# Kernel optimization log

Measured on AMD Instinct MI355X. Metric: run time of the kernel, lower is better.

The kernel has to match this reference:

```python
import jax, jax.numpy as jnp
import numpy as np

N = 100000
E = 1600000
IN_C = 128
OUT_C = 32
HEADS = 4
NEG_SLOPE = 0.2


def setup_inputs() -> dict:
    key = jax.random.key(0)
    k1, k2, k3, k4, k5 = jax.random.split(key, 5)
    x = jax.random.normal(k1, (N, IN_C), dtype=jnp.float32)
    edge_index = jax.random.randint(k2, (2, E), 0, N, dtype=jnp.int64)
    # Xavier-ish scaled params
    W = jax.random.normal(k3, (OUT_C * HEADS, IN_C), dtype=jnp.float32) * (1.414 * np.sqrt(2.0 / (IN_C + OUT_C * HEADS)))
    att_l = jax.random.normal(k4, (1, HEADS, OUT_C), dtype=jnp.float32) * 0.1
    att_r = jax.random.normal(k5, (1, HEADS, OUT_C), dtype=jnp.float32) * 0.1
    bias = jnp.zeros((OUT_C * HEADS,), dtype=jnp.float32)
    return {"x": x, "edge_index": edge_index, "W": W, "att_l": att_l, "att_r": att_r, "bias": bias}


def reference(x, edge_index, W, att_l, att_r, bias):
    row, col = edge_index[0], edge_index[1]
    # per-node projection: [N, H, C]
    x_proj = (x @ W.T).reshape(N, HEADS, OUT_C)
    x_i = x_proj[row]          # [E, H, C] gather by source
    x_j = x_proj[col]          # [E, H, C] gather by target
    alpha = (x_i * att_l).sum(-1) + (x_j * att_r).sum(-1)   # [E, H]
    alpha = jnp.where(alpha >= 0, alpha, NEG_SLOPE * alpha)  # leaky_relu
    # edge softmax grouped by row (faithful: plain exp, eps=1e-16)
    alpha_exp = jnp.exp(alpha)
    denom = jax.ops.segment_sum(alpha_exp, row, num_segments=N)  # [N, H]
    alpha = alpha_exp / (denom[row] + 1e-16)
    # weighted scatter-add over all heads at once: [N, H, C]
    out = jax.ops.segment_sum(x_j * alpha[:, :, None], row, num_segments=N)
    out = out.reshape(N, HEADS * OUT_C) + bias
    return out
```

## Files before the change

kernel.cpp:

```cpp
#include <hip/hip_runtime.h>
#include <hip/hip_fp16.h>


constexpr float NEG_SLOPE = 0.2f;
constexpr int TILE_ROWS = 64;
constexpr int SLAB = 2048;
constexpr int EPB = 8192;
constexpr int NB_PAD = 2048;
constexpr int FBMAX = 256;

typedef __attribute__((ext_vector_type(8))) short short8;
typedef __attribute__((ext_vector_type(4))) float f32x4;

__device__ inline short f2bf(float f) {
    unsigned u = __float_as_uint(f);
    return (short)((u + 0x7fffu + ((u >> 16) & 1u)) >> 16);
}

__global__ __launch_bounds__(512) void k_fg(const float* __restrict__ x,
                                            const float* __restrict__ W,
                                            const float* __restrict__ attl,
                                            const float* __restrict__ attr,
                                            const int* __restrict__ ei,
                                            __half* __restrict__ xph,
                                            float* __restrict__ l,
                                            float* __restrict__ r,
                                            unsigned int* __restrict__ slab,
                                            int* __restrict__ starts,
                                            int N, int E, int NB, int FB, int S) {
    __shared__ __align__(16) char smem[49152];
    __shared__ float s_att[256];
    __shared__ int s_wsum[8];
    int t = threadIdx.x;
    int lane = t & 63, wv = t >> 6;
    int b = blockIdx.x;
    bool isfill = (b % S == 0) && (b / S < FB);

    if (isfill) {
        int* s_hist = (int*)smem;
        int* s_cur  = (int*)(smem + 8192);
        unsigned int* s_stage = (unsigned int*)(smem + 16384);

        int fb = b / S;
        int e0 = fb * EPB;
        int ecnt = min(EPB, E - e0);
        bool full = (ecnt == EPB) && ((E & 3) == 0);

        for (int i = t; i < NB_PAD; i += 512) s_hist[i] = 0;
        __syncthreads();

        const int* rows = ei;
        const int* cols = ei + E;

        if (full) {
            const int4* r4 = (const int4*)rows + (e0 >> 2);
#pragma unroll
            for (int k = 0; k < 4; ++k) {
                int4 ra = r4[k * 512 + t];
                atomicAdd(&s_hist[ra.x >> 6], 1);
                atomicAdd(&s_hist[ra.y >> 6], 1);
                atomicAdd(&s_hist[ra.z >> 6], 1);
                atomicAdd(&s_hist[ra.w >> 6], 1);
            }
        } else {
            for (int j = t; j < ecnt; j += 512)
                atomicAdd(&s_hist[rows[e0 + j] >> 6], 1);
        }
        __syncthreads();

        int b0 = t * 4;
        int c0 = s_hist[b0], c1 = s_hist[b0 + 1], c2 = s_hist[b0 + 2], c3 = s_hist[b0 + 3];
        int p = c0 + c1 + c2 + c3;
        int v = p;
#pragma unroll
        for (int off = 1; off < 64; off <<= 1) {
            int u = __shfl_up(v, off);
            if (lane >= off) v += u;
        }
        if (lane == 63) s_wsum[wv] = v;
        __syncthreads();
        if (t == 0) {
            int run = 0;
#pragma unroll
            for (int w = 0; w < 8; ++w) { int tmp = s_wsum[w]; s_wsum[w] = run; run += tmp; }
        }
        __syncthreads();
        int base = s_wsum[wv] + (v - p);
        int e1 = base + c0, e2 = e1 + c1, e3 = e2 + c2;
        s_hist[b0] = base; s_hist[b0 + 1] = e1; s_hist[b0 + 2] = e2; s_hist[b0 + 3] = e3;
        s_cur[b0] = base;  s_cur[b0 + 1] = e1;  s_cur[b0 + 2] = e2;  s_cur[b0 + 3] = e3;
        size_t sb = (size_t)fb * (NB + 1);
        if (b0 + 0 <= NB) starts[sb + b0 + 0] = base;
        if (b0 + 1 <= NB) starts[sb + b0 + 1] = e1;
        if (b0 + 2 <= NB) starts[sb + b0 + 2] = e2;
        if (b0 + 3 <= NB) starts[sb + b0 + 3] = e3;
        __syncthreads();

        if (full) {
            const int4* r4 = (const int4*)rows + (e0 >> 2);
            const int4* c4 = (const int4*)cols + (e0 >> 2);
#pragma unroll
            for (int k = 0; k < 4; ++k) {
                int4 ra = r4[k * 512 + t];
                int4 ca = c4[k * 512 + t];
                int pos;
                pos = atomicAdd(&s_cur[ra.x >> 6], 1);
                s_stage[pos] = ((unsigned int)ca.x << 6) | (unsigned int)(ra.x & 63);
                pos = atomicAdd(&s_cur[ra.y >> 6], 1);
                s_stage[pos] = ((unsigned int)ca.y << 6) | (unsigned int)(ra.y & 63);
                pos = atomicAdd(&s_cur[ra.z >> 6], 1);
                s_stage[pos] = ((unsigned int)ca.z << 6) | (unsigned int)(ra.z & 63);
                pos = atomicAdd(&s_cur[ra.w >> 6], 1);
                s_stage[pos] = ((unsigned int)ca.w << 6) | (unsigned int)(ra.w & 63);
            }
        } else {
            for (int j = t; j < ecnt; j += 512) {
                int rr = rows[e0 + j], cc = cols[e0 + j];
                int pos = atomicAdd(&s_cur[rr >> 6], 1);
                s_stage[pos] = ((unsigned int)cc << 6) | (unsigned int)(rr & 63);
            }
        }
        __syncthreads();

        uint4* dst = (uint4*)(slab + (size_t)fb * EPB);
        const uint4* src = (const uint4*)s_stage;
        int n4 = (ecnt + 3) >> 2;
        for (int i = t; i < n4; i += 512) dst[i] = src[i];
        return;
    }

    short* s_wa = (short*)smem;
    if (t < 128)       s_att[t] = attl[t];
    else if (t < 256)  s_att[t] = attr[t - 128];
    for (int i = t; i < 128 * 128; i += 512) {
        int row = i >> 7, col = i & 127;
        s_wa[row * 136 + col] = f2bf(W[i]);
    }
    for (int i = t; i < 1024; i += 512) {
        int row = 136 + (i >> 7), col = i & 127;
        s_wa[row * 136 + col] = 0;
    }
    __syncthreads();
#pragma unroll
    for (int s = 0; s < 2; ++s) {
        int e = t + s * 512;
        int which = e >> 9;
        int h = (e >> 7) & 3;
        int k = e & 127;
        float acc = 0.f;
#pragma unroll 8
        for (int c = 0; c < 32; ++c)
            acc += s_att[which * 128 + h * 32 + c] * W[(h * 32 + c) * 128 + k];
        s_wa[(128 + which * 4 + h) * 136 + k] = f2bf(acc);
    }
    __syncthreads();

    int li = lane & 15, quad = lane >> 4;
    int gb = b - min((b + S - 1) / S, FB);
    int base = gb * 128 + wv * 16;

    f32x4 acc[9];
#pragma unroll
    for (int nt = 0; nt < 9; ++nt) acc[nt] = (f32x4){0.f, 0.f, 0.f, 0.f};

    int anode = base + li;
    bool avalid = anode < N;
    const float4* x4 = (const float4*)x;
    const short8* wb8 = (const short8*)s_wa;

#pragma unroll
    for (int kc = 0; kc < 4; ++kc) {
        float4 p0 = make_float4(0.f, 0.f, 0.f, 0.f), p1 = p0;
        if (avalid) {
            p0 = x4[(size_t)anode * 32 + kc * 8 + quad * 2];
            p1 = x4[(size_t)anode * 32 + kc * 8 + quad * 2 + 1];
        }
        short8 a;
        a[0] = f2bf(p0.x); a[1] = f2bf(p0.y); a[2] = f2bf(p0.z); a[3] = f2bf(p0.w);
        a[4] = f2bf(p1.x); a[5] = f2bf(p1.y); a[6] = f2bf(p1.z); a[7] = f2bf(p1.w);
#pragma unroll
        for (int nt = 0; nt < 9; ++nt) {
            short8 bfrag = wb8[(nt * 16 + li) * 17 + kc * 4 + quad];
            acc[nt] = __builtin_amdgcn_mfma_f32_16x16x32_bf16(a, bfrag, acc[nt], 0, 0, 0);
        }
    }

#pragma unroll
    for (int j = 0; j < 4; ++j) {
        int node = base + quad * 4 + j;
        if (node >= N) continue;
        if (li < 4)      l[node * 4 + li] = acc[8][j];
        else if (li < 8) r[node * 4 + li - 4] = acc[8][j];
    }

    __syncthreads();
    __half* s_out = (__half*)s_wa;
#pragma unroll
    for (int j = 0; j < 4; ++j) {
        int nl = wv * 16 + quad * 4 + j;
#pragma unroll
        for (int nt = 0; nt < 8; ++nt)
            s_out[nl * 136 + nt * 16 + li] = __float2half(acc[nt][j]);
    }
    __syncthreads();
    {
        int nl = t >> 2, seg = t & 3;
        int node = gb * 128 + nl;
        if (node < N) {
            const short8* sr = (const short8*)s_wa;
            short8* xp8 = (short8*)xph;
#pragma unroll
            for (int q = 0; q < 4; ++q)
                xp8[(size_t)node * 16 + seg * 4 + q] = sr[nl * 17 + seg * 4 + q];
        }
    }
}

__global__ __launch_bounds__(512, 8) void k_tile(const int* __restrict__ starts,
                                                 const unsigned int* __restrict__ slab,
                                                 const float* __restrict__ l,
                                                 const float* __restrict__ r,
                                                 const __half* __restrict__ xph,
                                                 const float* __restrict__ bias,
                                                 float* __restrict__ out,
                                                 int N, int NB, int FB) {
    __shared__ int s_col[SLAB];
    __shared__ __half s_w[SLAB * 4];
    __shared__ float s_dsum[TILE_ROWS * 4];
    __shared__ float s_l[TILE_ROWS * 4];
    __shared__ int s_start[TILE_ROWS + 1];
    __shared__ int s_cursor[TILE_ROWS];
    __shared__ int s_cnt[TILE_ROWS];
    __shared__ int s_fbase[FBMAX];
    __shared__ int s_foff[FBMAX + 1];
    __shared__ int s_w4[4];

    int b = blockIdx.x;
    int base = b * TILE_ROWS;
    int t = threadIdx.x;
    int lane = t & 63, wv = t >> 6;
    int rows = min(TILE_ROWS, N - base);

    if (t < TILE_ROWS) s_cnt[t] = 0;
    if (t < rows * 4) s_l[t] = l[base * 4 + t];

    int myc = 0;
    if (t < FB) {
        const int* sp = starts + (size_t)t * (NB + 1) + b;
        int a0 = sp[0], a1 = sp[1];
        s_fbase[t] = a0;
        myc = a1 - a0;
    }
    if (t < 256) {
        int v = myc;
#pragma unroll
        for (int off = 1; off < 64; off <<= 1) {
            int u = __shfl_up(v, off);
            if (lane >= off) v += u;
        }
        if (lane == 63) s_w4[wv] = v;
        s_foff[t + 1] = v;
    }
    __syncthreads();
    if (t == 0) {
        int run = 0;
#pragma unroll
        for (int w = 0; w < 4; ++w) { int tmp = s_w4[w]; s_w4[w] = run; run += tmp; }
        s_foff[0] = 0;
    }
    __syncthreads();
    if (t < 256) s_foff[t + 1] += s_w4[wv];
    __syncthreads();
    int tot = s_foff[FB];
    if (tot > SLAB) tot = SLAB;

    unsigned int pk[4];
#pragma unroll
    for (int s = 0; s < 4; ++s) {
        int i = t + s * 512;
        pk[s] = 0xFFFFFFFFu;
        if (i < tot) {
            int lo = 0, hi = FB;
            while (hi - lo > 1) {
                int mid = (lo + hi) >> 1;
                if (s_foff[mid] <= i) lo = mid; else hi = mid;
            }
            pk[s] = slab[(size_t)lo * EPB + s_fbase[lo] + (i - s_foff[lo])];
        }
    }
#pragma unroll
    for (int s = 0; s < 4; ++s)
        if (pk[s] != 0xFFFFFFFFu) atomicAdd(&s_cnt[pk[s] & 63], 1);
    __syncthreads();

    if (t < 64) {
        int c = s_cnt[t];
        int vv = c;
#pragma unroll
        for (int off = 1; off < 64; off <<= 1) {
            int u = __shfl_up(vv, off);
            if (t >= off) vv += u;
        }
        s_start[t + 1] = vv;
        if (t == 0) s_start[0] = 0;
        s_cursor[t] = vv - c;
    }
    __syncthreads();

    {
        int row_[4], col_[4];
#pragma unroll
        for (int s = 0; s < 4; ++s) {
            row_[s] = (int)(pk[s] & 63);
            col_[s] = (pk[s] != 0xFFFFFFFFu) ? (int)(pk[s] >> 6) : 0;
        }
        float4 rv[4];
#pragma unroll
        for (int s = 0; s < 4; ++s) rv[s] = ((const float4*)r)[col_[s]];
#pragma unroll
        for (int s = 0; s < 4; ++s) {
            if (pk[s] == 0xFFFFFFFFu) continue;
            int row = row_[s];
            int pos = atomicAdd(&s_cursor[row], 1);
            s_col[pos] = col_[s];
            float4 lv = ((const float4*)s_l)[row];
            float w0 = lv.x + rv[s].x, w1 = lv.y + rv[s].y;
            float w2 = lv.z + rv[s].z, w3 = lv.w + rv[s].w;
            w0 = w0 >= 0.f ? w0 : NEG_SLOPE * w0;
            w1 = w1 >= 0.f ? w1 : NEG_SLOPE * w1;
            w2 = w2 >= 0.f ? w2 : NEG_SLOPE * w2;
            w3 = w3 >= 0.f ? w3 : NEG_SLOPE * w3;
            w0 = __expf(w0); w1 = __expf(w1); w2 = __expf(w2); w3 = __expf(w3);
            ((__half2*)s_w)[pos * 2]     = __floats2half2_rn(w0, w1);
            ((__half2*)s_w)[pos * 2 + 1] = __floats2half2_rn(w2, w3);
        }
    }
    __syncthreads();

    if (t < 256) {
        int row = t >> 2, h = t & 3;
        if (row < rows) {
            int s0 = s_start[row], s1 = s_start[row + 1];
            float d = 0.f;
            for (int i = s0; i < s1; ++i)
                d += __half2float(s_w[i * 4 + h]);
            s_dsum[t] = d;
        }
    }
    __syncthreads();

    int quarter = lane >> 4;
    int li = lane & 15;
    int h = li >> 2;
    const float4* xp4g = (const float4*)xph;

    float4 b0 = ((const float4*)bias)[2 * li];
    float4 b1 = ((const float4*)bias)[2 * li + 1];

    for (int rl = wv; rl < rows; rl += 8) {
        int s0 = s_start[rl], s1 = s_start[rl + 1];
        float a0 = 0.f, a1 = 0.f, a2 = 0.f, a3 = 0.f;
        float a4 = 0.f, a5 = 0.f, a6 = 0.f, a7 = 0.f;
        for (int i0 = s0 + quarter; i0 < s1; i0 += 16) {
            int i1 = i0 + 4, i2 = i0 + 8, i3 = i0 + 12;
            bool v1 = i1 < s1, v2 = i2 < s1, v3 = i3 < s1;
            int c0 = s_col[i0];
            int c1 = v1 ? s_col[i1] : c0;
            int c2 = v2 ? s_col[i2] : c0;
            int c3 = v3 ? s_col[i3] : c0;
            float w0 = __half2float(s_w[i0 * 4 + h]);
            float w1 = v1 ? __half2float(s_w[i1 * 4 + h]) : 0.f;
            float w2 = v2 ? __half2float(s_w[i2 * 4 + h]) : 0.f;
            float w3 = v3 ? __half2float(s_w[i3 * 4 + h]) : 0.f;
            float4 r0 = xp4g[(size_t)c0 * 16 + li];
            float4 r1 = xp4g[(size_t)c1 * 16 + li];
            float4 r2 = xp4g[(size_t)c2 * 16 + li];
            float4 r3 = xp4g[(size_t)c3 * 16 + li];
#define ACC8(raw, w)                                             \
            {                                                    \
                const __half* hp = (const __half*)&(raw);        \
                a0 = fmaf((w), __half2float(hp[0]), a0);         \
                a1 = fmaf((w), __half2float(hp[1]), a1);         \
                a2 = fmaf((w), __half2float(hp[2]), a2);         \
                a3 = fmaf((w), __half2float(hp[3]), a3);         \
                a4 = fmaf((w), __half2float(hp[4]), a4);         \
                a5 = fmaf((w), __half2float(hp[5]), a5);         \
                a6 = fmaf((w), __half2float(hp[6]), a6);         \
                a7 = fmaf((w), __half2float(hp[7]), a7);         \
            }
            ACC8(r0, w0);
            ACC8(r1, w1);
            ACC8(r2, w2);
            ACC8(r3, w3);
#undef ACC8
        }
        a0 += __shfl_xor(a0, 16); a0 += __shfl_xor(a0, 32);
        a1 += __shfl_xor(a1, 16); a1 += __shfl_xor(a1, 32);
        a2 += __shfl_xor(a2, 16); a2 += __shfl_xor(a2, 32);
        a3 += __shfl_xor(a3, 16); a3 += __shfl_xor(a3, 32);
        a4 += __shfl_xor(a4, 16); a4 += __shfl_xor(a4, 32);
        a5 += __shfl_xor(a5, 16); a5 += __shfl_xor(a5, 32);
        a6 += __shfl_xor(a6, 16); a6 += __shfl_xor(a6, 32);
        a7 += __shfl_xor(a7, 16); a7 += __shfl_xor(a7, 32);
        if (quarter == 0) {
            float inv = 1.f / (s_dsum[rl * 4 + h] + 1e-16f);
            float4 o0, o1;
            o0.x = a0 * inv + b0.x; o0.y = a1 * inv + b0.y;
            o0.z = a2 * inv + b0.z; o0.w = a3 * inv + b0.w;
            o1.x = a4 * inv + b1.x; o1.y = a5 * inv + b1.y;
            o1.z = a6 * inv + b1.z; o1.w = a7 * inv + b1.w;
            ((float4*)out)[(size_t)(base + rl) * 32 + 2 * li] = o0;
            ((float4*)out)[(size_t)(base + rl) * 32 + 2 * li + 1] = o1;
        }
    }
}

extern "C" void kernel_launch(void* const* d_in, const int* in_sizes, int n_in,
                              void* d_out, int out_size, void* d_ws, size_t ws_size,
                              hipStream_t stream) {
    const float* x    = (const float*)d_in[0];
    const int*   ei   = (const int*)d_in[1];
    const float* W    = (const float*)d_in[2];
    const float* attl = (const float*)d_in[3];
    const float* attr = (const float*)d_in[4];
    const float* bias = (const float*)d_in[5];
    int N = in_sizes[0] / 128;
    int E = in_sizes[1] / 2;
    int NB = (N + TILE_ROWS - 1) / TILE_ROWS;
    int FB = (E + EPB - 1) / EPB;

    char* ws = (char*)d_ws;
    __half* xph = (__half*)ws;   ws += (size_t)N * 128 * 2;
    float* l    = (float*)ws;    ws += (size_t)N * 4 * 4;
    float* r    = (float*)ws;    ws += (size_t)N * 4 * 4;
    int* starts = (int*)ws;      ws += (size_t)FB * (NB + 1) * 4;
    unsigned int* slab = (unsigned int*)ws; ws += (size_t)FB * EPB * 4;

    float* out = (float*)d_out;
    int GB = (N + 127) / 128;
    int TOT = FB + GB;
    int S = TOT / FB; if (S < 1) S = 1;

    k_fg<<<TOT, 512, 0, stream>>>(x, W, attl, attr, ei, xph, l, r, slab, starts,
                                  N, E, NB, FB, S);
    k_tile<<<NB, 512, 0, stream>>>(starts, slab, l, r, xph, bias, out, N, NB, FB);
}
```

Baseline: 206.7 us.

## Sub-sort tile edges by row and coarse column bucket for gather locality

After: 208.8 us. Within noise of the previous version (+1.0%).

```diff
diff --git a/kernel.cpp b/kernel.cpp
--- a/kernel.cpp
+++ b/kernel.cpp
@@ -5,6 +5,7 @@
 constexpr float NEG_SLOPE = 0.2f;
 constexpr int TILE_ROWS = 64;
 constexpr int SLAB = 2048;
+constexpr int KEYS = 1024;
 constexpr int EPB = 8192;
 constexpr int NB_PAD = 2048;
 constexpr int FBMAX = 256;
@@ -216,24 +217,24 @@
     }
 }
 
-__global__ __launch_bounds__(512, 8) void k_tile(const int* __restrict__ starts,
-                                                 const unsigned int* __restrict__ slab,
-                                                 const float* __restrict__ l,
-                                                 const float* __restrict__ r,
-                                                 const __half* __restrict__ xph,
-                                                 const float* __restrict__ bias,
-                                                 float* __restrict__ out,
-                                                 int N, int NB, int FB) {
+__global__ __launch_bounds__(512) void k_tile(const int* __restrict__ starts,
+                                              const unsigned int* __restrict__ slab,
+                                              const float* __restrict__ l,
+                                              const float* __restrict__ r,
+                                              const __half* __restrict__ xph,
+                                              const float* __restrict__ bias,
+                                              float* __restrict__ out,
+                                              int N, int NB, int FB, int tshift) {
     __shared__ int s_col[SLAB];
     __shared__ __half s_w[SLAB * 4];
+    __shared__ int s_kcnt[KEYS];
     __shared__ float s_dsum[TILE_ROWS * 4];
     __shared__ float s_l[TILE_ROWS * 4];
     __shared__ int s_start[TILE_ROWS + 1];
-    __shared__ int s_cursor[TILE_ROWS];
-    __shared__ int s_cnt[TILE_ROWS];
     __shared__ int s_fbase[FBMAX];
     __shared__ int s_foff[FBMAX + 1];
     __shared__ int s_w4[4];
+    __shared__ int s_w8[8];
 
     int b = blockIdx.x;
     int base = b * TILE_ROWS;
@@ -241,7 +242,7 @@
     int lane = t & 63, wv = t >> 6;
     int rows = min(TILE_ROWS, N - base);
 
-    if (t < TILE_ROWS) s_cnt[t] = 0;
+    for (int i = t; i < KEYS; i += 512) s_kcnt[i] = 0;
     if (t < rows * 4) s_l[t] = l[base * 4 + t];
 
     int myc = 0;
@@ -290,20 +291,35 @@
     }
 #pragma unroll
     for (int s = 0; s < 4; ++s)
-        if (pk[s] != 0xFFFFFFFFu) atomicAdd(&s_cnt[pk[s] & 63], 1);
-    __syncthreads();
-
-    if (t < 64) {
-        int c = s_cnt[t];
-        int vv = c;
+        if (pk[s] != 0xFFFFFFFFu) {
+            int key = ((int)(pk[s] & 63) << 4) | ((int)(pk[s] >> 6) >> tshift);
+            atomicAdd(&s_kcnt[key], 1);
+        }
+    __syncthreads();
+
+    {
+        int b0 = t * 2;
+        int c0 = s_kcnt[b0], c1 = s_kcnt[b0 + 1];
+        int p = c0 + c1;
+        int v = p;
 #pragma unroll
         for (int off = 1; off < 64; off <<= 1) {
-            int u = __shfl_up(vv, off);
-            if (t >= off) vv += u;
-        }
-        s_start[t + 1] = vv;
-        if (t == 0) s_start[0] = 0;
-        s_cursor[t] = vv - c;
+            int u = __shfl_up(v, off);
+            if (lane >= off) v += u;
+        }
+        if (lane == 63) s_w8[wv] = v;
+        __syncthreads();
+        if (t == 0) {
+            int run = 0;
+#pragma unroll
+            for (int w = 0; w < 8; ++w) { int tmp = s_w8[w]; s_w8[w] = run; run += tmp; }
+        }
+        __syncthreads();
+        int kbase = s_w8[wv] + (v - p);
+        s_kcnt[b0] = kbase;
+        s_kcnt[b0 + 1] = kbase + c0;
+        if ((b0 & 15) == 0) s_start[b0 >> 4] = kbase;
+        if (t == 511) s_start[64] = kbase + p;
     }
     __syncthreads();
 
@@ -321,7 +337,8 @@
         for (int s = 0; s < 4; ++s) {
             if (pk[s] == 0xFFFFFFFFu) continue;
             int row = row_[s];
-            int pos = atomicAdd(&s_cursor[row], 1);
+            int key = (row << 4) | (col_[s] >> tshift);
+            int pos = atomicAdd(&s_kcnt[key], 1);
             s_col[pos] = col_[s];
             float4 lv = ((const float4*)s_l)[row];
             float w0 = lv.x + rv[s].x, w1 = lv.y + rv[s].y;
@@ -441,7 +458,10 @@
     int TOT = FB + GB;
     int S = TOT / FB; if (S < 1) S = 1;
 
+    int tshift = 0;
+    while (((N - 1) >> tshift) >= 16) tshift++;
+
     k_fg<<<TOT, 512, 0, stream>>>(x, W, attl, attr, ei, xph, l, r, slab, starts,
                                   N, E, NB, FB, S);
-    k_tile<<<NB, 512, 0, stream>>>(starts, slab, l, r, xph, bias, out, N, NB, FB);
+    k_tile<<<NB, 512, 0, stream>>>(starts, slab, l, r, xph, bias, out, N, NB, FB, tshift);
 }
```
